# Optimization experiments

Measured on AMD Instinct MI355X. Metric: run time of the kernel, lower is better.

## Reference

```python
import jax, jax.numpy as jnp
import numpy as np

EPS = 1e-8  # torch nn.CosineSimilarity default eps


def setup_inputs() -> dict:
    key = jax.random.key(0)
    k1, k2 = jax.random.split(key)
    text_encodings = jax.random.normal(k1, (65536, 256), dtype=jnp.float32)
    label_encodings = jax.random.normal(k2, (1024, 256), dtype=jnp.float32)
    return {"text_encodings": text_encodings, "label_encodings": label_encodings}


def reference(text_encodings, label_encodings):
    # cosine_sim(x, y) = x.y / max(||x||*||y||, eps), computed as one matmul
    dots = jnp.einsum('nd,ld->nl', text_encodings, label_encodings)  # [N, L]
    tn = jnp.linalg.norm(text_encodings, axis=-1)    # [N]
    ln = jnp.linalg.norm(label_encodings, axis=-1)   # [L]
    denom = jnp.maximum(tn[:, None] * ln[None, :], EPS)
    return dots / denom
```

## Files before the change

kernel.cpp:

```cpp
#include <hip/hip_runtime.h>
#include <hip/hip_bf16.h>

#define NT 65536
#define NL 1024
#define DD 256

#define BM 128
#define BN 128
#define BK 64

typedef __attribute__((ext_vector_type(4))) float f32x4;
typedef __attribute__((ext_vector_type(8))) short bf16x8;

__device__ inline short f2bf(float x) {
    union { __hip_bfloat16 b; short s; } u;
    u.b = __float2bfloat16(x);
    return u.s;
}

__device__ inline void gload_lds16(const void* g, void* l) {
    __builtin_amdgcn_global_load_lds((const __attribute__((address_space(1))) void*)g,
                                     (__attribute__((address_space(3))) void*)l,
                                     16, 0, 0);
}

__global__ __launch_bounds__(256) void prep_k(const float* __restrict__ A,
                                              const float* __restrict__ Bm,
                                              short* __restrict__ Abf,
                                              short* __restrict__ Bbf,
                                              float* __restrict__ rt,
                                              float* __restrict__ rl) {
    int gw   = (blockIdx.x * 256 + threadIdx.x) >> 6;
    int lane = threadIdx.x & 63;
    if (gw >= NT + NL) return;
    const float* src = (gw < NT) ? (A + (size_t)gw * DD) : (Bm + (size_t)(gw - NT) * DD);
    short*       dst = (gw < NT) ? (Abf + (size_t)gw * DD) : (Bbf + (size_t)(gw - NT) * DD);
    float4 v = reinterpret_cast<const float4*>(src)[lane];
    short4 o;
    o.x = f2bf(v.x); o.y = f2bf(v.y); o.z = f2bf(v.z); o.w = f2bf(v.w);
    reinterpret_cast<short4*>(dst)[lane] = o;
    float s = v.x * v.x + v.y * v.y + v.z * v.z + v.w * v.w;
#pragma unroll
    for (int off = 32; off > 0; off >>= 1) s += __shfl_xor(s, off);
    if (lane == 0) {
        float r = 1.0f / fmaxf(sqrtf(s), 1e-20f);
        if (gw < NT) rt[gw] = r; else rl[gw - NT] = r;
    }
}

__global__ __launch_bounds__(512, 4) void cosim_bf_k(const short* __restrict__ Abf,
                                                     const short* __restrict__ Bbf,
                                                     const float* __restrict__ rt,
                                                     const float* __restrict__ rl,
                                                     float* __restrict__ C) {
    __shared__ short As[2][BM * BK];
    __shared__ short Bs[2][BN * BK];

    const int tid  = threadIdx.x;
    const int lane = tid & 63;
    const int w    = tid >> 6;
    const int wr   = w >> 2;
    const int wc   = w & 3;

    const int orig = blockIdx.x;
    const int id   = (orig & 7) * (4096 / 8) + (orig >> 3);
    const int bx   = id & 7;
    const int by   = id >> 3;
    const int m0   = by * BM;
    const int l0   = bx * BN;

    const int l8 = lane >> 3;
    const int ch = lane & 7;
    const int cg = ch ^ l8;

    const int fr = lane & 15;
    const int fq = lane >> 4;

    f32x4 acc[4][2] = {};

    auto stage = [&](int kt, int p) {
#pragma unroll
        for (int i = 0; i < 2; ++i) {
            int slot  = w * 2 + i;
            int rbase = slot * 8;
            int r     = rbase + l8;
            gload_lds16(Abf + (size_t)(m0 + r) * DD + kt * BK + cg * 8,
                        &As[p][rbase * BK]);
            gload_lds16(Bbf + (size_t)(l0 + r) * DD + kt * BK + cg * 8,
                        &Bs[p][rbase * BK]);
        }
    };

    stage(0, 0);
    __syncthreads();
    int p = 0;
#pragma unroll
    for (int kt = 0; kt < DD / BK; ++kt) {
        if (kt < DD / BK - 1) stage(kt + 1, p ^ 1);
#pragma unroll
        for (int ks = 0; ks < 2; ++ks) {
            bf16x8 af[4], bfr[2];
#pragma unroll
            for (int i = 0; i < 4; ++i) {
                int row = wr * 64 + i * 16 + fr;
                int ck  = (ks * 4 + fq) ^ (row & 7);
                af[i] = *reinterpret_cast<const bf16x8*>(&As[p][row * BK + ck * 8]);
            }
#pragma unroll
            for (int j = 0; j < 2; ++j) {
                int row = wc * 32 + j * 16 + fr;
                int ck  = (ks * 4 + fq) ^ (row & 7);
                bfr[j] = *reinterpret_cast<const bf16x8*>(&Bs[p][row * BK + ck * 8]);
            }
#pragma unroll
            for (int i = 0; i < 4; ++i)
#pragma unroll
                for (int j = 0; j < 2; ++j)
                    acc[i][j] = __builtin_amdgcn_mfma_f32_16x16x32_bf16(
                        af[i], bfr[j], acc[i][j], 0, 0, 0);
        }
        if (kt < DD / BK - 1) __syncthreads();
        p ^= 1;
    }

    const int crow0 = m0 + wr * 64;
    const int ccol0 = l0 + wc * 32;
    const int rq = lane >> 4;
    const int cc = lane & 15;
#pragma unroll
    for (int i = 0; i < 4; ++i) {
#pragma unroll
        for (int r = 0; r < 4; ++r) {
            int row = crow0 + i * 16 + rq * 4 + r;
            float rsc = rt[row];
            float* crow = C + (size_t)row * NL;
#pragma unroll
            for (int j = 0; j < 2; ++j) {
                int col = ccol0 + j * 16 + cc;
                crow[col] = acc[i][j][r] * rsc * rl[col];
            }
        }
    }
}

__global__ __launch_bounds__(256) void norms_k(const float* __restrict__ A,
                                               const float* __restrict__ Bm,
                                               float* __restrict__ rt,
                                               float* __restrict__ rl) {
    int gw   = (blockIdx.x * 256 + threadIdx.x) >> 6;
    int lane = threadIdx.x & 63;
    if (gw >= NT + NL) return;
    const float* src = (gw < NT) ? (A + (size_t)gw * DD) : (Bm + (size_t)(gw - NT) * DD);
    float4 v = reinterpret_cast<const float4*>(src)[lane];
    float s = v.x * v.x + v.y * v.y + v.z * v.z + v.w * v.w;
#pragma unroll
    for (int off = 32; off > 0; off >>= 1) s += __shfl_xor(s, off);
    if (lane == 0) {
        float r = 1.0f / fmaxf(sqrtf(s), 1e-20f);
        if (gw < NT) rt[gw] = r; else rl[gw - NT] = r;
    }
}

__global__ __launch_bounds__(256, 2) void cosim_fused_k(const float* __restrict__ A,
                                                        const float* __restrict__ Bm,
                                                        const float* __restrict__ rt,
                                                        const float* __restrict__ rl,
                                                        float* __restrict__ C) {
    __shared__ short As[BM * BK];
    __shared__ short Bs[BN * BK];
    const int tid  = threadIdx.x;
    const int lane = tid & 63;
    const int wid  = tid >> 6;
    const int wr   = wid >> 1;
    const int wc   = wid & 1;
    const int orig = blockIdx.x;
    const int id   = (orig & 7) * (4096 / 8) + (orig >> 3);
    const int bx   = id & 7;
    const int by   = id >> 3;
    const int m0 = by * BM;
    const int l0 = bx * BN;
    const int srow = tid >> 4;
    const int sc4  = tid & 15;
    f32x4 ra[8], rb[8];
    auto loadg = [&](int kt) {
        const float* pa = A  + (size_t)m0 * DD + kt * BK;
        const float* pb = Bm + (size_t)l0 * DD + kt * BK;
#pragma unroll
        for (int i = 0; i < 8; ++i) {
            int row = srow + i * 16;
            ra[i] = reinterpret_cast<const f32x4*>(pa + (size_t)row * DD)[sc4];
            rb[i] = reinterpret_cast<const f32x4*>(pb + (size_t)row * DD)[sc4];
        }
    };
    auto stash = [&]() {
#pragma unroll
        for (int i = 0; i < 8; ++i) {
            int row = srow + i * 16;
            short4 pa, pb;
            pa.x = f2bf(ra[i].x); pa.y = f2bf(ra[i].y);
            pa.z = f2bf(ra[i].z); pa.w = f2bf(ra[i].w);
            pb.x = f2bf(rb[i].x); pb.y = f2bf(rb[i].y);
            pb.z = f2bf(rb[i].z); pb.w = f2bf(rb[i].w);
            *reinterpret_cast<short4*>(&As[row * BK + sc4 * 4]) = pa;
            *reinterpret_cast<short4*>(&Bs[row * BK + sc4 * 4]) = pb;
        }
    };
    f32x4 acc[4][4] = {};
    loadg(0);
#pragma unroll
    for (int kt = 0; kt < DD / BK; ++kt) {
        __syncthreads();
        stash();
        __syncthreads();
        if (kt < DD / BK - 1) loadg(kt + 1);
#pragma unroll
        for (int ks = 0; ks < 2; ++ks) {
            bf16x8 af[4], bfr[4];
            const int kof = ks * 32 + (lane >> 4) * 8;
            const int ar  = wr * 64 + (lane & 15);
            const int bc  = wc * 64 + (lane & 15);
#pragma unroll
            for (int i = 0; i < 4; ++i)
                af[i] = *reinterpret_cast<const bf16x8*>(&As[(ar + i * 16) * BK + kof]);
#pragma unroll
            for (int j = 0; j < 4; ++j)
                bfr[j] = *reinterpret_cast<const bf16x8*>(&Bs[(bc + j * 16) * BK + kof]);
#pragma unroll
            for (int i = 0; i < 4; ++i)
#pragma unroll
                for (int j = 0; j < 4; ++j)
                    acc[i][j] = __builtin_amdgcn_mfma_f32_16x16x32_bf16(
                        af[i], bfr[j], acc[i][j], 0, 0, 0);
        }
    }
    const int crow0 = m0 + wr * 64;
    const int ccol0 = l0 + wc * 64;
    const int rq = lane >> 4;
    const int cc = lane & 15;
#pragma unroll
    for (int i = 0; i < 4; ++i) {
#pragma unroll
        for (int r = 0; r < 4; ++r) {
            int row = crow0 + i * 16 + rq * 4 + r;
            float rsc = rt[row];
            float* crow = C + (size_t)row * NL;
#pragma unroll
            for (int j = 0; j < 4; ++j) {
                int col = ccol0 + j * 16 + cc;
                crow[col] = acc[i][j][r] * rsc * rl[col];
            }
        }
    }
}

extern "C" void kernel_launch(void* const* d_in, const int* in_sizes, int n_in,
                              void* d_out, int out_size, void* d_ws, size_t ws_size,
                              hipStream_t stream) {
    const float* A  = (const float*)d_in[0];
    const float* Bm = (const float*)d_in[1];
    float* C = (float*)d_out;

    const size_t abf_elems = (size_t)NT * DD;
    const size_t bbf_elems = (size_t)NL * DD;
    const size_t need = (abf_elems + bbf_elems) * sizeof(short)
                      + (NT + NL) * sizeof(float);

    if (ws_size >= need) {
        short* Abf = (short*)d_ws;
        short* Bbf = Abf + abf_elems;
        float* rt  = (float*)(Bbf + bbf_elems);
        float* rl  = rt + NT;
        prep_k<<<(NT + NL) / 4, 256, 0, stream>>>(A, Bm, Abf, Bbf, rt, rl);
        cosim_bf_k<<<(NL / BN) * (NT / BM), 512, 0, stream>>>(Abf, Bbf, rt, rl, C);
    } else {
        float* rt = (float*)d_ws;
        float* rl = rt + NT;
        norms_k<<<(NT + NL) / 4, 256, 0, stream>>>(A, Bm, rt, rl);
        cosim_fused_k<<<(NL / BN) * (NT / BM), 256, 0, stream>>>(A, Bm, rt, rl, C);
    }
}
```

Before: 345.8 us.

## Make bf16 cosine GEMM persistent with resident B tile and 4-stage A pipeline

Replaces the one-tile-per-block grid with 256 persistent blocks. Each block keeps its full 128x256 bf16 B tile resident in LDS and walks a strip of 16 consecutive 128-row A tiles. A is streamed through a 4-buffer LDS ring with manual vmcnt waits and raw barriers, and the row and column norm reciprocals are cached in LDS. The aim is to cut redundant B loads, per-block launch and prologue cost, and global norm reads. The trade-off is lower occupancy from the larger LDS footprint and fragile hand-tuned wait counts.

```diff
diff --git a/kernel.cpp b/kernel.cpp
--- a/kernel.cpp
+++ b/kernel.cpp
@@ -8,6 +8,7 @@
 #define BM 128
 #define BN 128
 #define BK 64
+#define TPB 16
 
 typedef __attribute__((ext_vector_type(4))) float f32x4;
 typedef __attribute__((ext_vector_type(8))) short bf16x8;
@@ -48,13 +49,15 @@
     }
 }
 
-__global__ __launch_bounds__(512, 4) void cosim_bf_k(const short* __restrict__ Abf,
+__global__ __launch_bounds__(512, 2) void cosim_bf_k(const short* __restrict__ Abf,
                                                      const short* __restrict__ Bbf,
                                                      const float* __restrict__ rt,
                                                      const float* __restrict__ rl,
                                                      float* __restrict__ C) {
-    __shared__ short As[2][BM * BK];
-    __shared__ short Bs[2][BN * BK];
+    __shared__ short Bs[BN * DD];
+    __shared__ short As[4][BM * BK];
+    __shared__ float rnA[TPB * BM];
+    __shared__ float rnB[BN];
 
     const int tid  = threadIdx.x;
     const int lane = tid & 63;
@@ -62,82 +65,115 @@
     const int wr   = w >> 2;
     const int wc   = w & 3;
 
-    const int orig = blockIdx.x;
-    const int id   = (orig & 7) * (4096 / 8) + (orig >> 3);
-    const int bx   = id & 7;
-    const int by   = id >> 3;
-    const int m0   = by * BM;
-    const int l0   = bx * BN;
-
-    const int l8 = lane >> 3;
-    const int ch = lane & 7;
-    const int cg = ch ^ l8;
+    const int xcd   = blockIdx.x & 7;
+    const int g2    = blockIdx.x >> 3;
+    const int bx    = g2 & 7;
+    const int sub   = g2 >> 3;
+    const int strip = xcd * 4 + sub;
+    const int m0b   = strip * (TPB * BM);
+    const int l0    = bx * BN;
+
+    {
+        const int r2 = lane >> 5;
+        const int ch = lane & 31;
+#pragma unroll
+        for (int i = 0; i < 8; ++i) {
+            int rbase = w * 16 + i * 2;
+            int row   = rbase + r2;
+            int cg    = ch ^ (row & 7);
+            gload_lds16(Bbf + (size_t)(l0 + row) * DD + cg * 8, &Bs[rbase * DD]);
+        }
+    }
+#pragma unroll
+    for (int i = 0; i < 4; ++i) {
+        int r = tid + i * 512;
+        rnA[r] = rt[m0b + r];
+    }
+    if (tid < BN) rnB[tid] = rl[l0 + tid];
+    __syncthreads();
+
+    const int r8  = lane >> 3;
+    const int ch8 = lane & 7;
+    const int cg8 = ch8 ^ r8;
+    auto stageA = [&](int g) {
+        const short* base = Abf + (size_t)(m0b + (g >> 2) * BM) * DD + (g & 3) * BK;
+        short* dst = As[g & 3];
+#pragma unroll
+        for (int i = 0; i < 2; ++i) {
+            int rbase = w * 16 + i * 8;
+            gload_lds16(base + (size_t)(rbase + r8) * DD + cg8 * 8, &dst[rbase * BK]);
+        }
+    };
+
+    stageA(0);
+    stageA(1);
 
     const int fr = lane & 15;
     const int fq = lane >> 4;
-
-    f32x4 acc[4][2] = {};
-
-    auto stage = [&](int kt, int p) {
-#pragma unroll
-        for (int i = 0; i < 2; ++i) {
-            int slot  = w * 2 + i;
-            int rbase = slot * 8;
-            int r     = rbase + l8;
-            gload_lds16(Abf + (size_t)(m0 + r) * DD + kt * BK + cg * 8,
-                        &As[p][rbase * BK]);
-            gload_lds16(Bbf + (size_t)(l0 + r) * DD + kt * BK + cg * 8,
-                        &Bs[p][rbase * BK]);
-        }
-    };
-
-    stage(0, 0);
-    __syncthreads();
-    int p = 0;
-#pragma unroll
-    for (int kt = 0; kt < DD / BK; ++kt) {
-        if (kt < DD / BK - 1) stage(kt + 1, p ^ 1);
-#pragma unroll
-        for (int ks = 0; ks < 2; ++ks) {
-            bf16x8 af[4], bfr[2];
-#pragma unroll
-            for (int i = 0; i < 4; ++i) {
-                int row = wr * 64 + i * 16 + fr;
-                int ck  = (ks * 4 + fq) ^ (row & 7);
-                af[i] = *reinterpret_cast<const bf16x8*>(&As[p][row * BK + ck * 8]);
+    const int cc = lane & 15;
+
+#pragma unroll 1
+    for (int t = 0; t < TPB; ++t) {
+        f32x4 acc[4][2] = {};
+#pragma unroll
+        for (int kt = 0; kt < 4; ++kt) {
+            const int g = t * 4 + kt;
+            if (kt == 0) {
+                stageA(g + 2);
+                if (t == 0) asm volatile("s_waitcnt vmcnt(4)" ::: "memory");
+                else        asm volatile("s_waitcnt vmcnt(36)" ::: "memory");
+            } else if (kt == 1) {
+                stageA(g + 2);
+                if (t == 0) asm volatile("s_waitcnt vmcnt(4)" ::: "memory");
+                else        asm volatile("s_waitcnt vmcnt(34)" ::: "memory");
+            } else if (kt == 2) {
+                if (t < TPB - 1) { stageA(g + 2); asm volatile("s_waitcnt vmcnt(4)" ::: "memory"); }
+                else             { asm volatile("s_waitcnt vmcnt(2)" ::: "memory"); }
+            } else {
+                if (t < TPB - 1) { stageA(g + 2); asm volatile("s_waitcnt vmcnt(4)" ::: "memory"); }
+                else             { asm volatile("s_waitcnt vmcnt(0)" ::: "memory"); }
             }
-#pragma unroll
-            for (int j = 0; j < 2; ++j) {
-                int row = wc * 32 + j * 16 + fr;
-                int ck  = (ks * 4 + fq) ^ (row & 7);
-                bfr[j] = *reinterpret_cast<const bf16x8*>(&Bs[p][row * BK + ck * 8]);
+            __builtin_amdgcn_s_barrier();
+
+            const short* A_ = As[g & 3];
+#pragma unroll
+            for (int ks = 0; ks < 2; ++ks) {
+                bf16x8 af[4], bf2[2];
+#pragma unroll
+                for (int i = 0; i < 4; ++i) {
+                    int row = wr * 64 + i * 16 + fr;
+                    int ck  = (ks * 4 + fq) ^ (row & 7);
+                    af[i] = *reinterpret_cast<const bf16x8*>(&A_[row * BK + ck * 8]);
+                }
+#pragma unroll
+                for (int j = 0; j < 2; ++j) {
+                    int row = wc * 32 + j * 16 + fr;
+                    int c   = kt * 8 + ks * 4 + fq;
+                    int ck  = c ^ (row & 7);
+                    bf2[j] = *reinterpret_cast<const bf16x8*>(&Bs[row * DD + ck * 8]);
+                }
+#pragma unroll
+                for (int i = 0; i < 4; ++i)
+#pragma unroll
+                    for (int j = 0; j < 2; ++j)
+                        acc[i][j] = __builtin_amdgcn_mfma_f32_16x16x32_bf16(
+                            af[i], bf2[j], acc[i][j], 0, 0, 0);
             }
-#pragma unroll
-            for (int i = 0; i < 4; ++i)
-#pragma unroll
-                for (int j = 0; j < 2; ++j)
-                    acc[i][j] = __builtin_amdgcn_mfma_f32_16x16x32_bf16(
-                        af[i], bfr[j], acc[i][j], 0, 0, 0);
-        }
-        if (kt < DD / BK - 1) __syncthreads();
-        p ^= 1;
-    }
-
-    const int crow0 = m0 + wr * 64;
-    const int ccol0 = l0 + wc * 32;
-    const int rq = lane >> 4;
-    const int cc = lane & 15;
-#pragma unroll
-    for (int i = 0; i < 4; ++i) {
-#pragma unroll
-        for (int r = 0; r < 4; ++r) {
-            int row = crow0 + i * 16 + rq * 4 + r;
-            float rsc = rt[row];
-            float* crow = C + (size_t)row * NL;
-#pragma unroll
-            for (int j = 0; j < 2; ++j) {
-                int col = ccol0 + j * 16 + cc;
-                crow[col] = acc[i][j][r] * rsc * rl[col];
+        }
+
+        const int m0 = m0b + t * BM;
+#pragma unroll
+        for (int i = 0; i < 4; ++i) {
+#pragma unroll
+            for (int rr = 0; rr < 4; ++rr) {
+                int lr = wr * 64 + i * 16 + fq * 4 + rr;
+                float rs = rnA[t * BM + lr];
+                float* crow = C + (size_t)(m0 + lr) * NL + l0;
+#pragma unroll
+                for (int j = 0; j < 2; ++j) {
+                    int lc = wc * 32 + j * 16 + cc;
+                    crow[lc] = acc[i][j][rr] * rs * rnB[lc];
+                }
             }
         }
     }
@@ -271,7 +307,7 @@
         float* rt  = (float*)(Bbf + bbf_elems);
         float* rl  = rt + NT;
         prep_k<<<(NT + NL) / 4, 256, 0, stream>>>(A, Bm, Abf, Bbf, rt, rl);
-        cosim_bf_k<<<(NL / BN) * (NT / BM), 512, 0, stream>>>(Abf, Bbf, rt, rl, C);
+        cosim_bf_k<<<256, 512, 0, stream>>>(Abf, Bbf, rt, rl, C);
     } else {
         float* rt = (float*)d_ws;
         float* rl = rt + NT;
```

Result: no change. 343.0 us (-0.8%).
